# Optimization experiments

Measured on AMD Instinct MI355X. Metric: run time of the kernel, lower is better.

## Reference

```python
import jax, jax.numpy as jnp
import numpy as np

WIDTH = 768
HEAD = 64

def setup_inputs() -> dict:
    key = jax.random.key(0)
    ks = jax.random.split(key, 8)
    x = jax.random.normal(ks[0], (8, 2048, WIDTH), dtype=jnp.float32)
    mask = jax.random.randint(ks[1], (2048, 2048), 0, 2, dtype=jnp.int32)
    s = 1.0 / np.sqrt(WIDTH)
    Wq = jax.random.normal(ks[2], (WIDTH, HEAD), dtype=jnp.float32) * s
    Wk = jax.random.normal(ks[3], (WIDTH, HEAD), dtype=jnp.float32) * s
    Wv = jax.random.normal(ks[4], (WIDTH, HEAD), dtype=jnp.float32) * s
    bq = jax.random.normal(ks[5], (HEAD,), dtype=jnp.float32) * 0.01
    bk = jax.random.normal(ks[6], (HEAD,), dtype=jnp.float32) * 0.01
    bv = jax.random.normal(ks[7], (HEAD,), dtype=jnp.float32) * 0.01
    return {"x": x, "Wq": Wq, "bq": bq, "Wk": Wk, "bk": bk, "Wv": Wv, "bv": bv, "mask": mask}

def reference(x, Wq, bq, Wk, bk, Wv, bv, mask) -> jnp.ndarray:
    # x: [B, N, width]; projections -> [B, N, head]
    Q = jnp.einsum('bnw,wh->bnh', x, Wq) + bq
    K = jnp.einsum('bnw,wh->bnh', x, Wk) + bk
    V = jnp.einsum('bnw,wh->bnh', x, Wv) + bv
    scale = 1.0 / jnp.sqrt(jnp.asarray(Q.shape[-1], dtype=Q.dtype))
    scores = jnp.einsum('bqh,bkh->bqk', Q, K) * scale  # [B, N, N]
    scores = jnp.where(mask == 0, -jnp.inf, scores)
    attn = jax.nn.softmax(scores, axis=-1)
    return jnp.einsum('bqk,bkh->bqh', attn, V)
```

## Files before the change

### kernel.cpp

```cpp
#include <hip/hip_runtime.h>

typedef short  s8v   __attribute__((ext_vector_type(8)));
typedef float  f32x4 __attribute__((ext_vector_type(4)));

#define SEQ 2048
#define WID 768

__device__ __forceinline__ unsigned fbits(float f) {
    union { float f; unsigned u; } v; v.f = f; return v.u;
}
__device__ __forceinline__ float bitsf(unsigned u) {
    union { unsigned u; float f; } v; v.u = u; return v.f;
}
__device__ __forceinline__ unsigned short f2b(float f) {
    unsigned u = fbits(f);
    return (unsigned short)((u + 0x7FFFu + ((u >> 16) & 1u)) >> 16);
}
__device__ __forceinline__ unsigned packRNE(float a, float b) {
    unsigned ta = fbits(a) + 0x7FFFu + ((fbits(a) >> 16) & 1u);
    unsigned tb = fbits(b) + 0x7FFFu + ((fbits(b) >> 16) & 1u);
    return __builtin_amdgcn_perm(tb, ta, 0x07060302u);
}
__device__ __forceinline__ unsigned packTRUNC(float a, float b) {
    return __builtin_amdgcn_perm(fbits(b), fbits(a), 0x07060302u);
}
__device__ __forceinline__ f32x4 zero4() { f32x4 z = {0.f, 0.f, 0.f, 0.f}; return z; }

__global__ __launch_bounds__(256) void convert_kernel(
    const int* __restrict__ mask,
    const float* __restrict__ Wq, const float* __restrict__ Wk, const float* __restrict__ Wv,
    unsigned* __restrict__ PM, unsigned short* __restrict__ WF)
{
    const int tid = threadIdx.x;
    const int blk = blockIdx.x;
    if (blk < 512) {
        const int gid  = blk * 4 + (tid >> 6);
        const int lane = tid & 63, quad = lane >> 4, c = lane & 15;
        const int qb = gid >> 5, kb = gid & 31;
        unsigned w = 0;
        #pragma unroll
        for (int mt = 0; mt < 2; ++mt)
            #pragma unroll
            for (int i = 0; i < 4; ++i) {
                const int q = qb * 32 + mt * 16 + quad * 4 + i;
                const int4 mm = *(const int4*)&mask[(size_t)q * SEQ + kb * 64 + 4 * c];
                if (mm.x) w |= 1u << (mt * 16 + i * 4 + 0);
                if (mm.y) w |= 1u << (mt * 16 + i * 4 + 1);
                if (mm.z) w |= 1u << (mt * 16 + i * 4 + 2);
                if (mm.w) w |= 1u << (mt * 16 + i * 4 + 3);
            }
        PM[(size_t)gid * 64 + lane] = w;
    } else {
        const int s2 = (blk - 512) * 256 + tid;
        const int chunk = s2 >> 6, l = s2 & 63;
        const int ntg = chunk / 24, r = chunk - ntg * 24;
        const int kc = r >> 1, h = r & 1;
        const int mat = ntg >> 2;
        const int col = (ntg & 3) * 16 + (l & 15);
        const int k0 = kc * 64 + h * 32 + (l >> 4) * 8;
        const float* Wm = (mat == 0) ? Wq : (mat == 1) ? Wk : Wv;
        float p[8];
        #pragma unroll
        for (int j = 0; j < 8; ++j) p[j] = Wm[(size_t)(k0 + j) * 64 + col];
        uint4 w;
        w.x = packRNE(p[0], p[1]); w.y = packRNE(p[2], p[3]);
        w.z = packRNE(p[4], p[5]); w.w = packRNE(p[6], p[7]);
        *(uint4*)&WF[(size_t)s2 * 8] = w;
    }
}

__global__ __launch_bounds__(256, 4) void qkv_proj_kernel(
    const float* __restrict__ x, const unsigned short* __restrict__ WF,
    const float* __restrict__ bq, const float* __restrict__ bk, const float* __restrict__ bv,
    unsigned short* __restrict__ QF, unsigned short* __restrict__ KF,
    unsigned short* __restrict__ VF)
{
    __shared__ unsigned short St[16][208];

    const int tid = threadIdx.x;
    const int wv = tid >> 6, lane = tid & 63, quad = lane >> 4, c = lane & 15;
    const int rowb = blockIdx.x * 16;
    const int c0w  = wv * 48;

    float bias[3];
    #pragma unroll
    for (int nt = 0; nt < 3; ++nt) {
        int col = c0w + nt * 16 + c;
        const float* B = (col < 64) ? bq : (col < 128) ? bk : bv;
        bias[nt] = B[col & 63];
    }

    const float* xrow = x + (size_t)(rowb + c) * WID + quad * 8;

    f32x4 acc[3];
    #pragma unroll
    for (int nt = 0; nt < 3; ++nt) acc[nt] = zero4();

    #pragma unroll
    for (int kc = 0; kc < 24; ++kc) {
        float4 f0 = *(const float4*)&xrow[kc * 32];
        float4 f1 = *(const float4*)&xrow[kc * 32 + 4];
        union { uint4 u; s8v v; } bf[3];
        #pragma unroll
        for (int nt = 0; nt < 3; ++nt) {
            const int ntg = wv * 3 + nt;
            bf[nt].u = *(const uint4*)&WF[(((size_t)ntg * 12 + (kc >> 1)) * 2 + (kc & 1)) * 512 + lane * 8];
        }
        union { uint4 u; s8v v; } af;
        af.u.x = packRNE(f0.x, f0.y);
        af.u.y = packRNE(f0.z, f0.w);
        af.u.z = packRNE(f1.x, f1.y);
        af.u.w = packRNE(f1.z, f1.w);
        #pragma unroll
        for (int nt = 0; nt < 3; ++nt)
            acc[nt] = __builtin_amdgcn_mfma_f32_16x16x32_bf16(af.v, bf[nt].v, acc[nt], 0, 0, 0);
    }

    #pragma unroll
    for (int nt = 0; nt < 3; ++nt)
        #pragma unroll
        for (int i = 0; i < 4; ++i)
            St[quad * 4 + i][c0w + nt * 16 + c] = f2b(acc[nt][i] + bias[nt]);
    __syncthreads();

    const int kb  = rowb >> 6;
    const int q0k = (rowb & 63) >> 2;
    const int ks0 = (rowb & 63) >> 5;
    const int qd0 = (rowb & 31) >> 3;

    if (tid < 128) {
        const int ks = tid >> 6, l = tid & 63, qd = l >> 4, cc = l & 15;
        uint4 v = *(uint4*)&St[cc][ks * 32 + qd * 8];
        *(uint4*)&QF[(((size_t)(rowb >> 4)) * 2 + ks) * 512 + (size_t)l * 8] = v;
    } else {
        const int u = tid - 128;
        const int ks = u >> 6, nt = (u >> 4) & 3, qd = (u >> 2) & 3, cc = u & 3;
        uint4 v = *(uint4*)&St[4 * cc + nt][64 + ks * 32 + qd * 8];
        *(uint4*)&KF[(((size_t)kb * 8 + ks * 4 + nt) * 64 + qd * 16 + q0k + cc) * 8] = v;
    }
    if (tid < 128) {
        const int d = tid >> 1, jj = tid & 1, qd = qd0 + jj;
        const int nt = d >> 4, cc = d & 15;
        unsigned short p[8];
        #pragma unroll
        for (int s = 0; s < 8; ++s) p[s] = St[jj * 8 + s][128 + d];
        uint4 w;
        w.x = (unsigned)p[0] | ((unsigned)p[1] << 16);
        w.y = (unsigned)p[2] | ((unsigned)p[3] << 16);
        w.z = (unsigned)p[4] | ((unsigned)p[5] << 16);
        w.w = (unsigned)p[6] | ((unsigned)p[7] << 16);
        *(uint4*)&VF[(((size_t)kb * 8 + ks0 * 4 + nt) * 64 + qd * 16 + cc) * 8] = w;
    }
}

__global__ __launch_bounds__(256, 4) void attn_kernel(
    const unsigned short* __restrict__ QF, const unsigned short* __restrict__ KF,
    const unsigned short* __restrict__ VF, const unsigned* __restrict__ PM,
    float* __restrict__ out)
{
    __shared__ unsigned short Ps[4][16][72];
    __shared__ float Obuf[16][68];
    __shared__ float Lbuf[16];

    const int tid = threadIdx.x;
    const int wv = tid >> 6, lane = tid & 63, quad = lane >> 4, c = lane & 15;
    const int blk = blockIdx.x;
    const int bb = blk & 7, g = blk >> 3;
    const int qb32 = g >> 1, mtq = g & 1;

    #pragma unroll
    for (int j = 0; j < 5; ++j) {
        int idx = tid + 256 * j;
        if (idx < 16 * 68) ((float*)Obuf)[idx] = 0.f;
    }
    if (tid < 16) Lbuf[tid] = 0.f;

    s8v qf[2];
    {
        const size_t qgrp = (size_t)bb * 128 + g;
        #pragma unroll
        for (int ks = 0; ks < 2; ++ks)
            qf[ks] = *(const s8v*)&QF[(qgrp * 2 + ks) * 512 + (size_t)lane * 8];
    }

    f32x4 O[4];
    float lro[4];
    #pragma unroll
    for (int nt = 0; nt < 4; ++nt) O[nt] = zero4();
    #pragma unroll
    for (int i = 0; i < 4; ++i) lro[i] = 0.f;

    #pragma unroll
    for (int kt = 0; kt < 8; ++kt) {
        const int kb = wv * 8 + kt;
        const size_t kbg = (size_t)bb * 32 + kb;
        const unsigned pm = PM[(size_t)(qb32 * 32 + kb) * 64 + lane];
        const unsigned pmh = pm >> (mtq * 16);

        f32x4 S[4];
        #pragma unroll
        for (int nt = 0; nt < 4; ++nt) S[nt] = zero4();
        {
            s8v kf[8];
            #pragma unroll
            for (int ch = 0; ch < 8; ++ch)
                kf[ch] = *(const s8v*)&KF[(kbg * 8 + ch) * 512 + (size_t)lane * 8];
            #pragma unroll
            for (int ks = 0; ks < 2; ++ks)
                #pragma unroll
                for (int nt = 0; nt < 4; ++nt)
                    S[nt] = __builtin_amdgcn_mfma_f32_16x16x32_bf16(qf[ks], kf[ks * 4 + nt], S[nt], 0, 0, 0);
        }

        s8v vf[8];
        #pragma unroll
        for (int ch = 0; ch < 8; ++ch)
            vf[ch] = *(const s8v*)&VF[(kbg * 8 + ch) * 512 + (size_t)lane * 8];

        #pragma unroll
        for (int i = 0; i < 4; ++i) {
            float p4[4];
            #pragma unroll
            for (int nt = 0; nt < 4; ++nt) {
                float e = exp2f(fmaf(S[nt][i], 0.18033688011112042f, -21.640425613334451f));
                p4[nt] = ((pmh >> (i * 4 + nt)) & 1u) ? e : 0.f;
            }
            unsigned u0 = packTRUNC(p4[0], p4[1]);
            unsigned u1 = packTRUNC(p4[2], p4[3]);
            lro[i] += bitsf(u0 << 16) + bitsf(u0 & 0xFFFF0000u)
                    + bitsf(u1 << 16) + bitsf(u1 & 0xFFFF0000u);
            *(uint2*)&Ps[wv][quad * 4 + i][4 * c] = make_uint2(u0, u1);
        }

        #pragma unroll
        for (int ks = 0; ks < 2; ++ks) {
            s8v a = *(const s8v*)&Ps[wv][c][ks * 32 + quad * 8];
            #pragma unroll
            for (int nt = 0; nt < 4; ++nt)
                O[nt] = __builtin_amdgcn_mfma_f32_16x16x32_bf16(a, vf[ks * 4 + nt], O[nt], 0, 0, 0);
        }
    }

    __syncthreads();
    #pragma unroll
    for (int i = 0; i < 4; ++i) {
        float l = lro[i];
        l += __shfl_xor(l, 1);
        l += __shfl_xor(l, 2);
        l += __shfl_xor(l, 4);
        l += __shfl_xor(l, 8);
        if (c == 0) atomicAdd(&Lbuf[quad * 4 + i], l);
        #pragma unroll
        for (int nt = 0; nt < 4; ++nt)
            atomicAdd(&Obuf[quad * 4 + i][nt * 16 + c], O[nt][i]);
    }
    __syncthreads();
    {
        const int r = tid >> 4, d4 = (tid & 15) * 4;
        const float invL = 1.0f / Lbuf[r];
        float4 v = *(float4*)&Obuf[r][d4];
        float4 o = make_float4(v.x * invL, v.y * invL, v.z * invL, v.w * invL);
        *(float4*)&out[((size_t)bb * SEQ + g * 16 + r) * 64 + d4] = o;
    }
}

extern "C" void kernel_launch(void* const* d_in, const int* in_sizes, int n_in,
                              void* d_out, int out_size, void* d_ws, size_t ws_size,
                              hipStream_t stream)
{
    const float* x    = (const float*)d_in[0];
    const float* Wq   = (const float*)d_in[1];
    const float* bq   = (const float*)d_in[2];
    const float* Wk   = (const float*)d_in[3];
    const float* bk   = (const float*)d_in[4];
    const float* Wv   = (const float*)d_in[5];
    const float* bv   = (const float*)d_in[6];
    const int*   mask = (const int*)d_in[7];
    float* out = (float*)d_out;

    unsigned short* QF = (unsigned short*)d_ws;
    unsigned short* KF = QF + (size_t)16384 * 64;
    unsigned short* VF = KF + (size_t)16384 * 64;
    unsigned short* WF = VF + (size_t)16384 * 64;
    unsigned*       PM = (unsigned*)(WF + (size_t)192 * WID);

    convert_kernel<<<584, 256, 0, stream>>>(mask, Wq, Wk, Wv, PM, WF);
    qkv_proj_kernel<<<1024, 256, 0, stream>>>(x, WF, bq, bk, bv, QF, KF, VF);
    attn_kernel<<<1024, 256, 0, stream>>>(QF, KF, VF, PM, out);
}
```

Baseline: 174.4 us.

## Stage QKV projection through double-buffered async LDS loads and prefetch K/V in attention

The projection kernel now processes 64 rows per 512-thread block, staging x and bf16 weight tiles into LDS with asynchronous global-to-LDS loads and double buffering. This lets each weight fragment serve two row tiles instead of being reloaded by every 16-row block. The attention kernel software-pipelines its K, V and mask loads one key block ahead, at the cost of more registers, and its occupancy hint drops to 2. The convert kernel is split into separate mask and weight kernels, which adds one extra launch.

After: 191.2 us. +9.6%, slower.

```diff
diff --git a/kernel.cpp b/kernel.cpp
--- a/kernel.cpp
+++ b/kernel.cpp
@@ -26,134 +26,181 @@
 }
 __device__ __forceinline__ f32x4 zero4() { f32x4 z = {0.f, 0.f, 0.f, 0.f}; return z; }
 
-__global__ __launch_bounds__(256) void convert_kernel(
-    const int* __restrict__ mask,
+__device__ __forceinline__ void async16(const unsigned short* g, void* l) {
+    __builtin_amdgcn_global_load_lds(
+        (const __attribute__((address_space(1))) unsigned int*)g,
+        (__attribute__((address_space(3))) unsigned int*)l, 16, 0, 0);
+}
+__device__ __forceinline__ void async16f(const float* g, void* l) {
+    __builtin_amdgcn_global_load_lds(
+        (const __attribute__((address_space(1))) unsigned int*)g,
+        (__attribute__((address_space(3))) unsigned int*)l, 16, 0, 0);
+}
+
+__global__ __launch_bounds__(256) void convert_mask_kernel(
+    const int* __restrict__ mask, unsigned* __restrict__ PM)
+{
+    const int tid = threadIdx.x;
+    const int gid  = blockIdx.x * 4 + (tid >> 6);
+    const int lane = tid & 63, quad = lane >> 4, c = lane & 15;
+    const int qb = gid >> 5, kb = gid & 31;
+    unsigned w = 0;
+    #pragma unroll
+    for (int mt = 0; mt < 2; ++mt)
+        #pragma unroll
+        for (int i = 0; i < 4; ++i) {
+            const int q = qb * 32 + mt * 16 + quad * 4 + i;
+            const int4 mm = *(const int4*)&mask[(size_t)q * SEQ + kb * 64 + 4 * c];
+            if (mm.x) w |= 1u << (mt * 16 + i * 4 + 0);
+            if (mm.y) w |= 1u << (mt * 16 + i * 4 + 1);
+            if (mm.z) w |= 1u << (mt * 16 + i * 4 + 2);
+            if (mm.w) w |= 1u << (mt * 16 + i * 4 + 3);
+        }
+    PM[(size_t)gid * 64 + lane] = w;
+}
+
+__global__ __launch_bounds__(256) void convert_w_kernel(
     const float* __restrict__ Wq, const float* __restrict__ Wk, const float* __restrict__ Wv,
-    unsigned* __restrict__ PM, unsigned short* __restrict__ WF)
-{
-    const int tid = threadIdx.x;
-    const int blk = blockIdx.x;
-    if (blk < 512) {
-        const int gid  = blk * 4 + (tid >> 6);
-        const int lane = tid & 63, quad = lane >> 4, c = lane & 15;
-        const int qb = gid >> 5, kb = gid & 31;
-        unsigned w = 0;
-        #pragma unroll
-        for (int mt = 0; mt < 2; ++mt)
-            #pragma unroll
-            for (int i = 0; i < 4; ++i) {
-                const int q = qb * 32 + mt * 16 + quad * 4 + i;
-                const int4 mm = *(const int4*)&mask[(size_t)q * SEQ + kb * 64 + 4 * c];
-                if (mm.x) w |= 1u << (mt * 16 + i * 4 + 0);
-                if (mm.y) w |= 1u << (mt * 16 + i * 4 + 1);
-                if (mm.z) w |= 1u << (mt * 16 + i * 4 + 2);
-                if (mm.w) w |= 1u << (mt * 16 + i * 4 + 3);
-            }
-        PM[(size_t)gid * 64 + lane] = w;
-    } else {
-        const int s2 = (blk - 512) * 256 + tid;
-        const int chunk = s2 >> 6, l = s2 & 63;
-        const int ntg = chunk / 24, r = chunk - ntg * 24;
-        const int kc = r >> 1, h = r & 1;
-        const int mat = ntg >> 2;
-        const int col = (ntg & 3) * 16 + (l & 15);
-        const int k0 = kc * 64 + h * 32 + (l >> 4) * 8;
-        const float* Wm = (mat == 0) ? Wq : (mat == 1) ? Wk : Wv;
-        float p[8];
-        #pragma unroll
-        for (int j = 0; j < 8; ++j) p[j] = Wm[(size_t)(k0 + j) * 64 + col];
-        uint4 w;
-        w.x = packRNE(p[0], p[1]); w.y = packRNE(p[2], p[3]);
-        w.z = packRNE(p[4], p[5]); w.w = packRNE(p[6], p[7]);
-        *(uint4*)&WF[(size_t)s2 * 8] = w;
-    }
-}
-
-__global__ __launch_bounds__(256, 4) void qkv_proj_kernel(
+    unsigned short* __restrict__ WF)
+{
+    const int s2 = blockIdx.x * 256 + threadIdx.x;
+    const int chunk = s2 >> 6, l = s2 & 63;
+    const int ntg = chunk / 24, r = chunk - ntg * 24;
+    const int kc = r >> 1, h = r & 1;
+    const int mat = ntg >> 2;
+    const int col = (ntg & 3) * 16 + (l & 15);
+    const int k0 = kc * 64 + h * 32 + (l >> 4) * 8;
+    const float* Wm = (mat == 0) ? Wq : (mat == 1) ? Wk : Wv;
+    float p[8];
+    #pragma unroll
+    for (int j = 0; j < 8; ++j) p[j] = Wm[(size_t)(k0 + j) * 64 + col];
+    uint4 w;
+    w.x = packRNE(p[0], p[1]); w.y = packRNE(p[2], p[3]);
+    w.z = packRNE(p[4], p[5]); w.w = packRNE(p[6], p[7]);
+    *(uint4*)&WF[(size_t)s2 * 8] = w;
+}
+
+__global__ __launch_bounds__(512, 2) void qkv_proj_kernel(
     const float* __restrict__ x, const unsigned short* __restrict__ WF,
     const float* __restrict__ bq, const float* __restrict__ bk, const float* __restrict__ bv,
     unsigned short* __restrict__ QF, unsigned short* __restrict__ KF,
     unsigned short* __restrict__ VF)
 {
-    __shared__ unsigned short St[16][208];
+    __shared__ __align__(16) unsigned char SM[40960];
+    unsigned short (*St)[200] = (unsigned short(*)[200])SM;
 
     const int tid = threadIdx.x;
     const int wv = tid >> 6, lane = tid & 63, quad = lane >> 4, c = lane & 15;
-    const int rowb = blockIdx.x * 16;
-    const int c0w  = wv * 48;
+    const int rg = wv >> 2, cg = wv & 3;
+    const int rowb = blockIdx.x * 64;
 
     float bias[3];
     #pragma unroll
     for (int nt = 0; nt < 3; ++nt) {
-        int col = c0w + nt * 16 + c;
+        int col = cg * 48 + nt * 16 + c;
         const float* B = (col < 64) ? bq : (col < 128) ? bk : bv;
         bias[nt] = B[col & 63];
     }
 
-    const float* xrow = x + (size_t)(rowb + c) * WID + quad * 8;
-
-    f32x4 acc[3];
-    #pragma unroll
-    for (int nt = 0; nt < 3; ++nt) acc[nt] = zero4();
-
-    #pragma unroll
+    auto issue = [&](int kc, int b) {
+        unsigned char* base = SM + b * 20480;
+        #pragma unroll
+        for (int t0 = 0; t0 < 3; ++t0) {
+            const int t = wv + 8 * t0;
+            if (t < 8) {
+                const int g = t >> 1, j = t & 1;
+                const float* src = x + (size_t)(rowb + g * 16 + c) * WID
+                                     + kc * 32 + quad * 8 + j * 4;
+                async16f(src, base + (g * 2 + j) * 1024);
+            } else if (t < 20) {
+                const int i = t - 8;
+                const unsigned short* src =
+                    WF + (((size_t)i * 12 + (kc >> 1)) * 2 + (kc & 1)) * 512 + lane * 8;
+                async16(src, base + 8192 + i * 1024);
+            }
+        }
+    };
+
+    f32x4 acc[2][3];
+    #pragma unroll
+    for (int mt = 0; mt < 2; ++mt)
+        #pragma unroll
+        for (int nt = 0; nt < 3; ++nt) acc[mt][nt] = zero4();
+
+    issue(0, 0);
     for (int kc = 0; kc < 24; ++kc) {
-        float4 f0 = *(const float4*)&xrow[kc * 32];
-        float4 f1 = *(const float4*)&xrow[kc * 32 + 4];
-        union { uint4 u; s8v v; } bf[3];
-        #pragma unroll
-        for (int nt = 0; nt < 3; ++nt) {
-            const int ntg = wv * 3 + nt;
-            bf[nt].u = *(const uint4*)&WF[(((size_t)ntg * 12 + (kc >> 1)) * 2 + (kc & 1)) * 512 + lane * 8];
-        }
-        union { uint4 u; s8v v; } af;
-        af.u.x = packRNE(f0.x, f0.y);
-        af.u.y = packRNE(f0.z, f0.w);
-        af.u.z = packRNE(f1.x, f1.y);
-        af.u.w = packRNE(f1.z, f1.w);
+        const int b = kc & 1;
+        __syncthreads();
+        if (kc < 23) issue(kc + 1, b ^ 1);
+
+        const unsigned char* base = SM + b * 20480;
+        s8v af[2];
+        #pragma unroll
+        for (int mt = 0; mt < 2; ++mt) {
+            const int g = rg * 2 + mt;
+            float4 f0 = *(const float4*)(base + (g * 2 + 0) * 1024 + lane * 16);
+            float4 f1 = *(const float4*)(base + (g * 2 + 1) * 1024 + lane * 16);
+            union { uint4 u; s8v v; } a;
+            a.u.x = packRNE(f0.x, f0.y);
+            a.u.y = packRNE(f0.z, f0.w);
+            a.u.z = packRNE(f1.x, f1.y);
+            a.u.w = packRNE(f1.z, f1.w);
+            af[mt] = a.v;
+        }
+        s8v bf[3];
         #pragma unroll
         for (int nt = 0; nt < 3; ++nt)
-            acc[nt] = __builtin_amdgcn_mfma_f32_16x16x32_bf16(af.v, bf[nt].v, acc[nt], 0, 0, 0);
-    }
-
-    #pragma unroll
-    for (int nt = 0; nt < 3; ++nt)
-        #pragma unroll
-        for (int i = 0; i < 4; ++i)
-            St[quad * 4 + i][c0w + nt * 16 + c] = f2b(acc[nt][i] + bias[nt]);
+            bf[nt] = *(const s8v*)(base + 8192 + (cg * 3 + nt) * 1024 + lane * 16);
+        #pragma unroll
+        for (int mt = 0; mt < 2; ++mt)
+            #pragma unroll
+            for (int nt = 0; nt < 3; ++nt)
+                acc[mt][nt] = __builtin_amdgcn_mfma_f32_16x16x32_bf16(
+                    af[mt], bf[nt], acc[mt][nt], 0, 0, 0);
+    }
+
     __syncthreads();
-
-    const int kb  = rowb >> 6;
-    const int q0k = (rowb & 63) >> 2;
-    const int ks0 = (rowb & 63) >> 5;
-    const int qd0 = (rowb & 31) >> 3;
-
-    if (tid < 128) {
-        const int ks = tid >> 6, l = tid & 63, qd = l >> 4, cc = l & 15;
-        uint4 v = *(uint4*)&St[cc][ks * 32 + qd * 8];
-        *(uint4*)&QF[(((size_t)(rowb >> 4)) * 2 + ks) * 512 + (size_t)l * 8] = v;
-    } else {
-        const int u = tid - 128;
-        const int ks = u >> 6, nt = (u >> 4) & 3, qd = (u >> 2) & 3, cc = u & 3;
-        uint4 v = *(uint4*)&St[4 * cc + nt][64 + ks * 32 + qd * 8];
-        *(uint4*)&KF[(((size_t)kb * 8 + ks * 4 + nt) * 64 + qd * 16 + q0k + cc) * 8] = v;
-    }
-    if (tid < 128) {
-        const int d = tid >> 1, jj = tid & 1, qd = qd0 + jj;
-        const int nt = d >> 4, cc = d & 15;
+    #pragma unroll
+    for (int mt = 0; mt < 2; ++mt)
+        #pragma unroll
+        for (int nt = 0; nt < 3; ++nt)
+            #pragma unroll
+            for (int i = 0; i < 4; ++i)
+                St[rg * 32 + mt * 16 + quad * 4 + i][cg * 48 + nt * 16 + c]
+                    = f2b(acc[mt][nt][i] + bias[nt]);
+    __syncthreads();
+
+    const int blk = blockIdx.x;
+    const int g0 = blk * 4;
+    {
+        const int g = tid >> 7, ks = (tid >> 6) & 1, l = tid & 63;
+        uint4 v = *(uint4*)&St[g * 16 + (l & 15)][ks * 32 + (l >> 4) * 8];
+        *(uint4*)&QF[(((size_t)(g0 + g)) * 2 + ks) * 512 + (size_t)l * 8] = v;
+    }
+    {
+        const int ksnt = tid >> 6, l = tid & 63;
+        const int ks = ksnt >> 2, nt = ksnt & 3;
+        uint4 v = *(uint4*)&St[4 * (l & 15) + nt][64 + ks * 32 + (l >> 4) * 8];
+        *(uint4*)&KF[(((size_t)blk * 8 + ksnt) * 64 + l) * 8] = v;
+    }
+    {
+        const int ksnt = tid >> 6, l = tid & 63;
+        const int ks = ksnt >> 2, nt = ksnt & 3;
+        const int d = 128 + nt * 16 + (l & 15);
+        const int r0 = ks * 32 + (l >> 4) * 8;
         unsigned short p[8];
         #pragma unroll
-        for (int s = 0; s < 8; ++s) p[s] = St[jj * 8 + s][128 + d];
+        for (int s = 0; s < 8; ++s) p[s] = St[r0 + s][d];
         uint4 w;
         w.x = (unsigned)p[0] | ((unsigned)p[1] << 16);
         w.y = (unsigned)p[2] | ((unsigned)p[3] << 16);
         w.z = (unsigned)p[4] | ((unsigned)p[5] << 16);
         w.w = (unsigned)p[6] | ((unsigned)p[7] << 16);
-        *(uint4*)&VF[(((size_t)kb * 8 + ks0 * 4 + nt) * 64 + qd * 16 + cc) * 8] = w;
-    }
-}
-
-__global__ __launch_bounds__(256, 4) void attn_kernel(
+        *(uint4*)&VF[(((size_t)blk * 8 + ksnt) * 64 + l) * 8] = w;
+    }
+}
+
+__global__ __launch_bounds__(256, 2) void attn_kernel(
     const unsigned short* __restrict__ QF, const unsigned short* __restrict__ KF,
     const unsigned short* __restrict__ VF, const unsigned* __restrict__ PM,
     float* __restrict__ out)
@@ -190,33 +237,42 @@
     #pragma unroll
     for (int i = 0; i < 4; ++i) lro[i] = 0.f;
 
+    s8v kf[8], vf[8];
+    unsigned pm;
+    {
+        const size_t kbg = (size_t)bb * 32 + wv * 8;
+        #pragma unroll
+        for (int ch = 0; ch < 8; ++ch) {
+            kf[ch] = *(const s8v*)&KF[(kbg * 8 + ch) * 512 + (size_t)lane * 8];
+            vf[ch] = *(const s8v*)&VF[(kbg * 8 + ch) * 512 + (size_t)lane * 8];
+        }
+        pm = PM[(size_t)(qb32 * 32 + wv * 8) * 64 + lane];
+    }
+
     #pragma unroll
     for (int kt = 0; kt < 8; ++kt) {
-        const int kb = wv * 8 + kt;
-        const size_t kbg = (size_t)bb * 32 + kb;
-        const unsigned pm = PM[(size_t)(qb32 * 32 + kb) * 64 + lane];
+        s8v kfn[8], vfn[8];
+        unsigned pmn = 0;
+        if (kt < 7) {
+            const size_t kbgn = (size_t)bb * 32 + wv * 8 + kt + 1;
+            #pragma unroll
+            for (int ch = 0; ch < 8; ++ch) {
+                kfn[ch] = *(const s8v*)&KF[(kbgn * 8 + ch) * 512 + (size_t)lane * 8];
+                vfn[ch] = *(const s8v*)&VF[(kbgn * 8 + ch) * 512 + (size_t)lane * 8];
+            }
+            pmn = PM[(size_t)(qb32 * 32 + wv * 8 + kt + 1) * 64 + lane];
+        }
+
+        f32x4 S[4];
+        #pragma unroll
+        for (int nt = 0; nt < 4; ++nt) S[nt] = zero4();
+        #pragma unroll
+        for (int ks = 0; ks < 2; ++ks)
+            #pragma unroll
+            for (int nt = 0; nt < 4; ++nt)
+                S[nt] = __builtin_amdgcn_mfma_f32_16x16x32_bf16(qf[ks], kf[ks * 4 + nt], S[nt], 0, 0, 0);
+
         const unsigned pmh = pm >> (mtq * 16);
-
-        f32x4 S[4];
-        #pragma unroll
-        for (int nt = 0; nt < 4; ++nt) S[nt] = zero4();
-        {
-            s8v kf[8];
-            #pragma unroll
-            for (int ch = 0; ch < 8; ++ch)
-                kf[ch] = *(const s8v*)&KF[(kbg * 8 + ch) * 512 + (size_t)lane * 8];
-            #pragma unroll
-            for (int ks = 0; ks < 2; ++ks)
-                #pragma unroll
-                for (int nt = 0; nt < 4; ++nt)
-                    S[nt] = __builtin_amdgcn_mfma_f32_16x16x32_bf16(qf[ks], kf[ks * 4 + nt], S[nt], 0, 0, 0);
-        }
-
-        s8v vf[8];
-        #pragma unroll
-        for (int ch = 0; ch < 8; ++ch)
-            vf[ch] = *(const s8v*)&VF[(kbg * 8 + ch) * 512 + (size_t)lane * 8];
-
         #pragma unroll
         for (int i = 0; i < 4; ++i) {
             float p4[4];
@@ -239,6 +295,10 @@
             for (int nt = 0; nt < 4; ++nt)
                 O[nt] = __builtin_amdgcn_mfma_f32_16x16x32_bf16(a, vf[ks * 4 + nt], O[nt], 0, 0, 0);
         }
+
+        #pragma unroll
+        for (int ch = 0; ch < 8; ++ch) { kf[ch] = kfn[ch]; vf[ch] = vfn[ch]; }
+        pm = pmn;
     }
 
     __syncthreads();
@@ -284,7 +344,8 @@
     unsigned short* WF = VF + (size_t)16384 * 64;
     unsigned*       PM = (unsigned*)(WF + (size_t)192 * WID);
 
-    convert_kernel<<<584, 256, 0, stream>>>(mask, Wq, Wk, Wv, PM, WF);
-    qkv_proj_kernel<<<1024, 256, 0, stream>>>(x, WF, bq, bk, bv, QF, KF, VF);
+    convert_mask_kernel<<<512, 256, 0, stream>>>(mask, PM);
+    convert_w_kernel<<<72, 256, 0, stream>>>(Wq, Wk, Wv, WF);
+    qkv_proj_kernel<<<256, 512, 0, stream>>>(x, WF, bq, bk, bv, QF, KF, VF);
     attn_kernel<<<1024, 256, 0, stream>>>(QF, KF, VF, PM, out);
 }
```
